# Optimization experiments

Measured on AMD Instinct MI355X. Metric: run time of the kernel, lower is better.

## Reference

```python
import jax, jax.numpy as jnp
import numpy as np

K = 8       # out_caps
H = 64      # nhidden
TAU = 1.0

def _l2norm(x, eps=1e-12):
    n = jnp.linalg.norm(x, axis=-1, keepdims=True)
    return x / jnp.maximum(n, eps)

def setup_inputs() -> dict:
    key = jax.random.key(0)
    k1, k2, k3, k4 = jax.random.split(key, 4)
    B, N, NB, D = 128, 50, 32, K * H
    return {
        "self_vectors": jax.random.normal(k1, (B, N, D), dtype=jnp.float32),
        "neighbor_vectors": jax.random.normal(k2, (B, N, NB, D), dtype=jnp.float32),
        "W1": jax.random.normal(k3, (D, D), dtype=jnp.float32) * 0.04,
        "b1": jax.random.normal(k4, (D,), dtype=jnp.float32) * 0.01,
        "max_iter": 3,
    }

def reference(self_vectors, neighbor_vectors, W1, b1, max_iter):
    B, N, _ = self_vectors.shape
    NB = neighbor_vectors.shape[2]
    # fc1 + ReLU projections (dropout p=0 -> identity)
    self_z = jax.nn.relu(self_vectors @ W1.T + b1)            # [B,N,K*H]
    neigh_z = jax.nn.relu(neighbor_vectors @ W1.T + b1)       # [B,N,NB,K*H]
    s = _l2norm(self_z.reshape(B, N, K, H))                   # [B,N,K,H]
    nz = _l2norm(neigh_z.reshape(B, N, NB, K, H))             # [B,N,NB,K,H]
    u = None
    for it in range(max_iter):
        if u is None:
            p = jnp.zeros((B, N, NB, K), dtype=s.dtype)
        else:
            p = jnp.einsum('bnmkh,bnkh->bnmk', nz, u)
        p = jax.nn.softmax(p / TAU, axis=-1)                   # softmax over K
        u = jnp.einsum('bnmkh,bnmk->bnkh', nz, p) + s          # sum over neighbors
        if it < max_iter - 1:
            u = _l2norm(u)
    return jax.nn.relu(u.reshape(B, N, K * H))
```

## Files before the change

### kernel.cpp

```cpp
#include <hip/hip_runtime.h>
#include <hip/hip_bf16.h>


#define D_DIM 512
#define BM 64
#define BK 32
#define KSTEPS 16

typedef __attribute__((ext_vector_type(8))) short short8;
typedef __attribute__((ext_vector_type(4))) short short4v;
typedef __attribute__((ext_vector_type(4))) float f32x4;

static __device__ __forceinline__ short f2bf(float f) {
    __bf16 b = (__bf16)f;
    return __builtin_bit_cast(short, b);
}
static __device__ __forceinline__ float bf2f(short s) {
    unsigned u = ((unsigned)(unsigned short)s) << 16;
    return __builtin_bit_cast(float, u);
}
static __device__ __forceinline__ void gload_lds16(const void* g, void* l) {
    __builtin_amdgcn_global_load_lds(
        (const __attribute__((address_space(1))) void*)g,
        (__attribute__((address_space(3))) void*)l, 16, 0, 0);
}

__global__ __launch_bounds__(256) void wconv(const float* __restrict__ W,
                                             short* __restrict__ Wb) {
    const int i = (blockIdx.x * 256 + threadIdx.x) * 8;
    const float4 v0 = *reinterpret_cast<const float4*>(W + i);
    const float4 v1 = *reinterpret_cast<const float4*>(W + i + 4);
    short8 o;
    o[0] = f2bf(v0.x); o[1] = f2bf(v0.y); o[2] = f2bf(v0.z); o[3] = f2bf(v0.w);
    o[4] = f2bf(v1.x); o[5] = f2bf(v1.y); o[6] = f2bf(v1.z); o[7] = f2bf(v1.w);
    *reinterpret_cast<short8*>(Wb + i) = o;
}

template <bool FUSED>
__global__ __launch_bounds__(256, 2) void gemm_route(
    const float* __restrict__ A,
    const short* __restrict__ Wb,
    const float* __restrict__ bias,
    short* __restrict__ Zs,
    const short* __restrict__ S,
    const int* __restrict__ miter_ptr,
    float* __restrict__ out)
{
    __shared__ __align__(16) char smem[81920];
    float* const lAf32 = (float*)smem;
    short* const lB = (short*)(smem + 16384);

    const int t = threadIdx.x;
    const int lane = t & 63;
    const int wid = t >> 6;
    const size_t row0 = (size_t)blockIdx.x * BM;
    const int wc = wid * 128;

    const int cb = wc + (lane & 15);
    float bcol[8];
    #pragma unroll
    for (int n = 0; n < 8; ++n) bcol[n] = bias[cb + n * 16];
    int miter = 0;
    if (FUSED) miter = *miter_ptr;

    auto stage = [&](int step, int buf) {
        const int k0 = (step < KSTEPS ? step : 0) * BK;
        #pragma unroll
        for (int i = 0; i < 8; ++i) {
            const int c = wid * 8 + i;
            const int r = c * 16 + (lane >> 2);
            const int g = ((lane & 3) - (r >> 1)) & 3;
            gload_lds16(Wb + (size_t)r * D_DIM + k0 + g * 8,
                        lB + buf * 16384 + c * 512);
        }
        #pragma unroll
        for (int i = 0; i < 2; ++i) {
            const int c = wid * 2 + i;
            const int r = c * 8 + (lane >> 3);
            const int g = ((lane & 7) - 2 * (r & 3)) & 7;
            gload_lds16(A + (row0 + r) * D_DIM + k0 + g * 4,
                        lAf32 + buf * 2048 + c * 256);
        }
    };

    f32x4 acc[4][8] = {};
    auto compute = [&](int buf) {
        const int q = lane >> 4;
        short8 af[4], bfr[8];
        #pragma unroll
        for (int m = 0; m < 4; ++m) {
            const int r = m * 16 + (lane & 15);
            const float* ap = lAf32 + buf * 2048 + r * 32 + ((q + (r & 3)) & 3) * 8;
            const f32x4 a0 = *reinterpret_cast<const f32x4*>(ap);
            const f32x4 a1 = *reinterpret_cast<const f32x4*>(ap + 4);
            short8 f;
            f[0] = f2bf(a0[0]); f[1] = f2bf(a0[1]);
            f[2] = f2bf(a0[2]); f[3] = f2bf(a0[3]);
            f[4] = f2bf(a1[0]); f[5] = f2bf(a1[1]);
            f[6] = f2bf(a1[2]); f[7] = f2bf(a1[3]);
            af[m] = f;
        }
        #pragma unroll
        for (int n = 0; n < 8; ++n) {
            const int r = wc + n * 16 + (lane & 15);
            bfr[n] = *reinterpret_cast<const short8*>(
                lB + buf * 16384 + r * 32 + ((q + (r >> 1)) & 3) * 8);
        }
        #pragma unroll
        for (int m = 0; m < 4; ++m)
            #pragma unroll
            for (int n = 0; n < 8; ++n)
                acc[m][n] = __builtin_amdgcn_mfma_f32_16x16x32_bf16(
                    af[m], bfr[n], acc[m][n], 0, 0, 0);
    };

    stage(0, 0);
    stage(1, 1);
    asm volatile("s_waitcnt vmcnt(10)" ::: "memory");
    __builtin_amdgcn_s_barrier();
    #pragma unroll
    for (int tk = 0; tk < KSTEPS; ++tk) {
        compute(tk & 1);
        asm volatile("s_waitcnt lgkmcnt(0)" ::: "memory");
        __builtin_amdgcn_s_barrier();
        stage(tk + 2, tk & 1);
        asm volatile("s_waitcnt vmcnt(10)" ::: "memory");
        __builtin_amdgcn_s_barrier();
    }
    asm volatile("s_waitcnt vmcnt(0)" ::: "memory");
    __builtin_amdgcn_s_barrier();

    short* const zbuf = (short*)(smem + 16384);
    #pragma unroll
    for (int m = 0; m < 4; ++m) {
        #pragma unroll
        for (int r = 0; r < 4; ++r) {
            float v[8];
            float ssa = 0.0f, ssb = 0.0f;
            #pragma unroll
            for (int n = 0; n < 4; ++n) {
                v[n] = fmaxf(acc[m][n][r] + bcol[n], 0.0f);
                ssa = fmaf(v[n], v[n], ssa);
            }
            #pragma unroll
            for (int n = 4; n < 8; ++n) {
                v[n] = fmaxf(acc[m][n][r] + bcol[n], 0.0f);
                ssb = fmaf(v[n], v[n], ssb);
            }
            ssa += __shfl_xor(ssa, 1); ssb += __shfl_xor(ssb, 1);
            ssa += __shfl_xor(ssa, 2); ssb += __shfl_xor(ssb, 2);
            ssa += __shfl_xor(ssa, 4); ssb += __shfl_xor(ssb, 4);
            ssa += __shfl_xor(ssa, 8); ssb += __shfl_xor(ssb, 8);
            const float inva = 1.0f / fmaxf(sqrtf(ssa), 1e-12f);
            const float invb = 1.0f / fmaxf(sqrtf(ssb), 1e-12f);
            const int orow = m * 16 + (lane >> 4) * 4 + r;
            if (FUSED) {
                #pragma unroll
                for (int n = 0; n < 4; ++n)
                    zbuf[orow * D_DIM + cb + n * 16] = f2bf(v[n] * inva);
                #pragma unroll
                for (int n = 4; n < 8; ++n)
                    zbuf[orow * D_DIM + cb + n * 16] = f2bf(v[n] * invb);
            } else {
                #pragma unroll
                for (int n = 0; n < 4; ++n)
                    Zs[(row0 + orow) * D_DIM + cb + n * 16] = f2bf(v[n] * inva);
                #pragma unroll
                for (int n = 4; n < 8; ++n)
                    Zs[(row0 + orow) * D_DIM + cb + n * 16] = f2bf(v[n] * invb);
            }
        }
    }

    if (!FUSED) return;
    __syncthreads();

    float* const scratch = (float*)smem;
    const int tt = t & 127;
    const int ssid = t >> 7;
    const size_t site = (size_t)blockIdx.x * 2 + ssid;
    float* const u_ = scratch + ssid * 512;
    float* const p_ = (float*)(smem + 4096) + ssid * 256;
    const short* const zr = zbuf + ssid * 32 * D_DIM;

    const int e = tt * 4;
    const int go = tt >> 4;
    const short4v sv = *reinterpret_cast<const short4v*>(S + site * D_DIM + e);
    const float s0 = bf2f(sv[0]), s1 = bf2f(sv[1]);
    const float s2 = bf2f(sv[2]), s3 = bf2f(sv[3]);

    float v0, v1, v2, v3;
    {
        float a0 = 0, a1 = 0, a2 = 0, a3 = 0;
        for (int m = 0; m < 32; ++m) {
            const short4v z = *reinterpret_cast<const short4v*>(zr + m * D_DIM + e);
            a0 += bf2f(z[0]); a1 += bf2f(z[1]); a2 += bf2f(z[2]); a3 += bf2f(z[3]);
        }
        v0 = fmaf(a0, 0.125f, s0); v1 = fmaf(a1, 0.125f, s1);
        v2 = fmaf(a2, 0.125f, s2); v3 = fmaf(a3, 0.125f, s3);
    }

    const int dm = tt >> 2;
    const int ka = (tt & 3) * 2;

    for (int it = 1; it < miter; ++it) {
        float ssum = v0 * v0 + v1 * v1 + v2 * v2 + v3 * v3;
        ssum += __shfl_xor(ssum, 1);
        ssum += __shfl_xor(ssum, 2);
        ssum += __shfl_xor(ssum, 4);
        ssum += __shfl_xor(ssum, 8);
        const float inv = 1.0f / fmaxf(sqrtf(ssum), 1e-12f);
        v0 *= inv; v1 *= inv; v2 *= inv; v3 *= inv;
        *reinterpret_cast<float4*>(u_ + e) = make_float4(v0, v1, v2, v3);
        __syncthreads();

        const short* const za = zr + dm * D_DIM + ka * 64;
        const float* const ua = u_ + ka * 64;
        float da = 0, db = 0;
        #pragma unroll
        for (int j = 0; j < 8; ++j) {
            const int jj = ((j + (tt & 7)) & 7) * 8;
            const short8 zva = *reinterpret_cast<const short8*>(za + jj);
            const short8 zvb = *reinterpret_cast<const short8*>(za + 64 + jj);
            const f32x4 uA0 = *reinterpret_cast<const f32x4*>(ua + jj);
            const f32x4 uA1 = *reinterpret_cast<const f32x4*>(ua + jj + 4);
            const f32x4 uB0 = *reinterpret_cast<const f32x4*>(ua + 64 + jj);
            const f32x4 uB1 = *reinterpret_cast<const f32x4*>(ua + 64 + jj + 4);
            #pragma unroll
            for (int qq = 0; qq < 4; ++qq) {
                da = fmaf(bf2f(zva[qq]), uA0[qq], da);
                da = fmaf(bf2f(zva[qq + 4]), uA1[qq], da);
                db = fmaf(bf2f(zvb[qq]), uB0[qq], db);
                db = fmaf(bf2f(zvb[qq + 4]), uB1[qq], db);
            }
        }
        float mx = fmaxf(da, db);
        mx = fmaxf(mx, __shfl_xor(mx, 1));
        mx = fmaxf(mx, __shfl_xor(mx, 2));
        const float ea = __expf(da - mx), eb = __expf(db - mx);
        float sm_ = ea + eb;
        sm_ += __shfl_xor(sm_, 1);
        sm_ += __shfl_xor(sm_, 2);
        const float rs = 1.0f / sm_;
        *reinterpret_cast<float2*>(p_ + dm * 8 + ka) = make_float2(ea * rs, eb * rs);
        __syncthreads();

        float a0 = 0, a1 = 0, a2 = 0, a3 = 0;
        for (int m = 0; m < 32; ++m) {
            const short4v z = *reinterpret_cast<const short4v*>(zr + m * D_DIM + e);
            const float pm = p_[m * 8 + go];
            a0 = fmaf(bf2f(z[0]), pm, a0); a1 = fmaf(bf2f(z[1]), pm, a1);
            a2 = fmaf(bf2f(z[2]), pm, a2); a3 = fmaf(bf2f(z[3]), pm, a3);
        }
        v0 = s0 + a0; v1 = s1 + a1; v2 = s2 + a2; v3 = s3 + a3;
    }

    *reinterpret_cast<float4*>(out + site * D_DIM + e) =
        make_float4(fmaxf(v0, 0.0f), fmaxf(v1, 0.0f),
                    fmaxf(v2, 0.0f), fmaxf(v3, 0.0f));
}

extern "C" void kernel_launch(void* const* d_in, const int* in_sizes, int n_in,
                              void* d_out, int out_size, void* d_ws, size_t ws_size,
                              hipStream_t stream) {
    const float* self_v  = (const float*)d_in[0];
    const float* neigh_v = (const float*)d_in[1];
    const float* W1      = (const float*)d_in[2];
    const float* b1      = (const float*)d_in[3];
    const int*   miter   = (const int*)d_in[4];
    float* out = (float*)d_out;

    const int sites = in_sizes[0] / D_DIM;
    const int nrows = in_sizes[1] / D_DIM;

    short* s  = (short*)d_ws;
    short* Wb = s + (size_t)sites * D_DIM;

    wconv<<<dim3(D_DIM * D_DIM / (256 * 8)), dim3(256), 0, stream>>>(W1, Wb);
    gemm_route<false><<<dim3(sites / BM), dim3(256), 0, stream>>>(
        self_v, Wb, b1, s, nullptr, nullptr, nullptr);
    gemm_route<true><<<dim3(nrows / BM), dim3(256), 0, stream>>>(
        neigh_v, Wb, b1, nullptr, s, miter, out);
}
```

Baseline: 250.5 us.

## Load GEMM operands directly into registers instead of staging through LDS

Drops the async global-to-LDS double-buffered staging of the A tile and the bf16 weights. Each lane now loads its MFMA fragments straight from global memory into a two-deep register buffer, prefetching the next K step while the current one computes. This removes LDS traffic, the swizzle arithmetic and the per-step barriers, and shrinks shared memory. In exchange it raises register pressure, duplicates global reads of W across blocks and waves with no LDS sharing, and uses less coalesced global access patterns.

```diff
diff --git a/kernel.cpp b/kernel.cpp
--- a/kernel.cpp
+++ b/kernel.cpp
@@ -4,7 +4,6 @@
 
 #define D_DIM 512
 #define BM 64
-#define BK 32
 #define KSTEPS 16
 
 typedef __attribute__((ext_vector_type(8))) short short8;
@@ -18,11 +17,6 @@
 static __device__ __forceinline__ float bf2f(short s) {
     unsigned u = ((unsigned)(unsigned short)s) << 16;
     return __builtin_bit_cast(float, u);
-}
-static __device__ __forceinline__ void gload_lds16(const void* g, void* l) {
-    __builtin_amdgcn_global_load_lds(
-        (const __attribute__((address_space(1))) void*)g,
-        (__attribute__((address_space(3))) void*)l, 16, 0, 0);
 }
 
 __global__ __launch_bounds__(256) void wconv(const float* __restrict__ W,
@@ -46,9 +40,7 @@
     const int* __restrict__ miter_ptr,
     float* __restrict__ out)
 {
-    __shared__ __align__(16) char smem[81920];
-    float* const lAf32 = (float*)smem;
-    short* const lB = (short*)(smem + 16384);
+    __shared__ __align__(16) char smem[71680];
 
     const int t = threadIdx.x;
     const int lane = t & 63;
@@ -63,74 +55,51 @@
     int miter = 0;
     if (FUSED) miter = *miter_ptr;
 
-    auto stage = [&](int step, int buf) {
-        const int k0 = (step < KSTEPS ? step : 0) * BK;
-        #pragma unroll
-        for (int i = 0; i < 8; ++i) {
-            const int c = wid * 8 + i;
-            const int r = c * 16 + (lane >> 2);
-            const int g = ((lane & 3) - (r >> 1)) & 3;
-            gload_lds16(Wb + (size_t)r * D_DIM + k0 + g * 8,
-                        lB + buf * 16384 + c * 512);
-        }
-        #pragma unroll
-        for (int i = 0; i < 2; ++i) {
-            const int c = wid * 2 + i;
-            const int r = c * 8 + (lane >> 3);
-            const int g = ((lane & 7) - 2 * (r & 3)) & 7;
-            gload_lds16(A + (row0 + r) * D_DIM + k0 + g * 4,
-                        lAf32 + buf * 2048 + c * 256);
-        }
+    const float* const aBase = A + (row0 + (lane & 15)) * D_DIM + (lane >> 4) * 8;
+    const short* const bBase = Wb + (size_t)(wc + (lane & 15)) * D_DIM + (lane >> 4) * 8;
+
+    float4 aR[2][8];
+    short8 bR[2][8];
+
+    auto loadStep = [&](int k0, int buf) {
+        #pragma unroll
+        for (int m = 0; m < 4; ++m) {
+            const float* p = aBase + m * 16 * D_DIM + k0;
+            aR[buf][2 * m]     = *reinterpret_cast<const float4*>(p);
+            aR[buf][2 * m + 1] = *reinterpret_cast<const float4*>(p + 4);
+        }
+        #pragma unroll
+        for (int n = 0; n < 8; ++n)
+            bR[buf][n] = *reinterpret_cast<const short8*>(bBase + n * 16 * D_DIM + k0);
     };
 
     f32x4 acc[4][8] = {};
-    auto compute = [&](int buf) {
-        const int q = lane >> 4;
-        short8 af[4], bfr[8];
+
+    loadStep(0, 0);
+    #pragma unroll
+    for (int tk = 0; tk < KSTEPS; ++tk) {
+        const int cur = tk & 1;
+        short8 af[4];
         #pragma unroll
         for (int m = 0; m < 4; ++m) {
-            const int r = m * 16 + (lane & 15);
-            const float* ap = lAf32 + buf * 2048 + r * 32 + ((q + (r & 3)) & 3) * 8;
-            const f32x4 a0 = *reinterpret_cast<const f32x4*>(ap);
-            const f32x4 a1 = *reinterpret_cast<const f32x4*>(ap + 4);
             short8 f;
-            f[0] = f2bf(a0[0]); f[1] = f2bf(a0[1]);
-            f[2] = f2bf(a0[2]); f[3] = f2bf(a0[3]);
-            f[4] = f2bf(a1[0]); f[5] = f2bf(a1[1]);
-            f[6] = f2bf(a1[2]); f[7] = f2bf(a1[3]);
+            #pragma unroll
+            for (int j = 0; j < 4; ++j) {
+                f[j]     = f2bf(aR[cur][2 * m][j]);
+                f[4 + j] = f2bf(aR[cur][2 * m + 1][j]);
+            }
             af[m] = f;
         }
-        #pragma unroll
-        for (int n = 0; n < 8; ++n) {
-            const int r = wc + n * 16 + (lane & 15);
-            bfr[n] = *reinterpret_cast<const short8*>(
-                lB + buf * 16384 + r * 32 + ((q + (r >> 1)) & 3) * 8);
-        }
+        if (tk < KSTEPS - 1) loadStep((tk + 1) * 32, cur ^ 1);
         #pragma unroll
         for (int m = 0; m < 4; ++m)
             #pragma unroll
             for (int n = 0; n < 8; ++n)
                 acc[m][n] = __builtin_amdgcn_mfma_f32_16x16x32_bf16(
-                    af[m], bfr[n], acc[m][n], 0, 0, 0);
-    };
-
-    stage(0, 0);
-    stage(1, 1);
-    asm volatile("s_waitcnt vmcnt(10)" ::: "memory");
-    __builtin_amdgcn_s_barrier();
-    #pragma unroll
-    for (int tk = 0; tk < KSTEPS; ++tk) {
-        compute(tk & 1);
-        asm volatile("s_waitcnt lgkmcnt(0)" ::: "memory");
-        __builtin_amdgcn_s_barrier();
-        stage(tk + 2, tk & 1);
-        asm volatile("s_waitcnt vmcnt(10)" ::: "memory");
-        __builtin_amdgcn_s_barrier();
-    }
-    asm volatile("s_waitcnt vmcnt(0)" ::: "memory");
-    __builtin_amdgcn_s_barrier();
-
-    short* const zbuf = (short*)(smem + 16384);
+                    af[m], bR[cur][n], acc[m][n], 0, 0, 0);
+    }
+
+    short* const zbuf = (short*)smem;
     #pragma unroll
     for (int m = 0; m < 4; ++m) {
         #pragma unroll
@@ -175,12 +144,11 @@
     if (!FUSED) return;
     __syncthreads();
 
-    float* const scratch = (float*)smem;
     const int tt = t & 127;
     const int ssid = t >> 7;
     const size_t site = (size_t)blockIdx.x * 2 + ssid;
-    float* const u_ = scratch + ssid * 512;
-    float* const p_ = (float*)(smem + 4096) + ssid * 256;
+    float* const u_ = (float*)(smem + 65536) + ssid * 512;
+    float* const p_ = (float*)(smem + 69632) + ssid * 256;
     const short* const zr = zbuf + ssid * 32 * D_DIM;
 
     const int e = tt * 4;
```

Result: slower. 552.7 us (+120.6%).

## Keep normalized neighbor projections in MFMA registers for routing instead of LDS

Applied to the files above, without the earlier changes.

The routing epilogue used to write the normalized bf16 projections to shared memory and re-read them in every iteration. It now keeps the fp32 normalized values in the MFMA accumulator registers. Dot products and weighted sums are done with wave shuffles, and only the routing logits go through LDS for the softmax. The change also raises wave priority around the MFMA block. This removes LDS round-trips and bf16 rounding of the projections, but adds shuffle reductions, a serial 64-thread softmax step and more barriers.

```diff
diff --git a/kernel.cpp b/kernel.cpp
--- a/kernel.cpp
+++ b/kernel.cpp
@@ -8,7 +8,6 @@
 #define KSTEPS 16
 
 typedef __attribute__((ext_vector_type(8))) short short8;
-typedef __attribute__((ext_vector_type(4))) short short4v;
 typedef __attribute__((ext_vector_type(4))) float f32x4;
 
 static __device__ __forceinline__ short f2bf(float f) {
@@ -55,8 +54,10 @@
     const int wid = t >> 6;
     const size_t row0 = (size_t)blockIdx.x * BM;
     const int wc = wid * 128;
-
-    const int cb = wc + (lane & 15);
+    const int l15 = lane & 15;
+    const int q = lane >> 4;
+
+    const int cb = wc + l15;
     float bcol[8];
     #pragma unroll
     for (int n = 0; n < 8; ++n) bcol[n] = bias[cb + n * 16];
@@ -85,12 +86,12 @@
 
     f32x4 acc[4][8] = {};
     auto compute = [&](int buf) {
-        const int q = lane >> 4;
+        const int sq = lane >> 4;
         short8 af[4], bfr[8];
         #pragma unroll
         for (int m = 0; m < 4; ++m) {
-            const int r = m * 16 + (lane & 15);
-            const float* ap = lAf32 + buf * 2048 + r * 32 + ((q + (r & 3)) & 3) * 8;
+            const int r = m * 16 + l15;
+            const float* ap = lAf32 + buf * 2048 + r * 32 + ((sq + (r & 3)) & 3) * 8;
             const f32x4 a0 = *reinterpret_cast<const f32x4*>(ap);
             const f32x4 a1 = *reinterpret_cast<const f32x4*>(ap + 4);
             short8 f;
@@ -102,16 +103,18 @@
         }
         #pragma unroll
         for (int n = 0; n < 8; ++n) {
-            const int r = wc + n * 16 + (lane & 15);
+            const int r = wc + n * 16 + l15;
             bfr[n] = *reinterpret_cast<const short8*>(
-                lB + buf * 16384 + r * 32 + ((q + (r >> 1)) & 3) * 8);
-        }
+                lB + buf * 16384 + r * 32 + ((sq + (r >> 1)) & 3) * 8);
+        }
+        __builtin_amdgcn_s_setprio(1);
         #pragma unroll
         for (int m = 0; m < 4; ++m)
             #pragma unroll
             for (int n = 0; n < 8; ++n)
                 acc[m][n] = __builtin_amdgcn_mfma_f32_16x16x32_bf16(
                     af[m], bfr[n], acc[m][n], 0, 0, 0);
+        __builtin_amdgcn_s_setprio(0);
     };
 
     stage(0, 0);
@@ -130,7 +133,6 @@
     asm volatile("s_waitcnt vmcnt(0)" ::: "memory");
     __builtin_amdgcn_s_barrier();
 
-    short* const zbuf = (short*)(smem + 16384);
     #pragma unroll
     for (int m = 0; m < 4; ++m) {
         #pragma unroll
@@ -153,15 +155,13 @@
             ssa += __shfl_xor(ssa, 8); ssb += __shfl_xor(ssb, 8);
             const float inva = 1.0f / fmaxf(sqrtf(ssa), 1e-12f);
             const float invb = 1.0f / fmaxf(sqrtf(ssb), 1e-12f);
-            const int orow = m * 16 + (lane >> 4) * 4 + r;
             if (FUSED) {
                 #pragma unroll
-                for (int n = 0; n < 4; ++n)
-                    zbuf[orow * D_DIM + cb + n * 16] = f2bf(v[n] * inva);
-                #pragma unroll
-                for (int n = 4; n < 8; ++n)
-                    zbuf[orow * D_DIM + cb + n * 16] = f2bf(v[n] * invb);
+                for (int n = 0; n < 4; ++n) acc[m][n][r] = v[n] * inva;
+                #pragma unroll
+                for (int n = 4; n < 8; ++n) acc[m][n][r] = v[n] * invb;
             } else {
+                const int orow = m * 16 + q * 4 + r;
                 #pragma unroll
                 for (int n = 0; n < 4; ++n)
                     Zs[(row0 + orow) * D_DIM + cb + n * 16] = f2bf(v[n] * inva);
@@ -173,91 +173,127 @@
     }
 
     if (!FUSED) return;
-    __syncthreads();
-
-    float* const scratch = (float*)smem;
-    const int tt = t & 127;
-    const int ssid = t >> 7;
-    const size_t site = (size_t)blockIdx.x * 2 + ssid;
-    float* const u_ = scratch + ssid * 512;
-    float* const p_ = (float*)(smem + 4096) + ssid * 256;
-    const short* const zr = zbuf + ssid * 32 * D_DIM;
-
-    const int e = tt * 4;
-    const int go = tt >> 4;
-    const short4v sv = *reinterpret_cast<const short4v*>(S + site * D_DIM + e);
-    const float s0 = bf2f(sv[0]), s1 = bf2f(sv[1]);
-    const float s2 = bf2f(sv[2]), s3 = bf2f(sv[3]);
-
-    float v0, v1, v2, v3;
+
+    float* const praw = (float*)smem;
+    const size_t site0 = (size_t)blockIdx.x * 2;
+
+    float sreg[2][8];
+    #pragma unroll
+    for (int st = 0; st < 2; ++st)
+        #pragma unroll
+        for (int n = 0; n < 8; ++n)
+            sreg[st][n] = bf2f(S[(site0 + st) * D_DIM + cb + n * 16]);
+
+    float u[2][8];
+    #pragma unroll
+    for (int st = 0; st < 2; ++st)
+        #pragma unroll
+        for (int n = 0; n < 8; ++n) {
+            float c = 0.0f;
+            #pragma unroll
+            for (int mi = 2 * st; mi < 2 * st + 2; ++mi)
+                #pragma unroll
+                for (int r = 0; r < 4; ++r) c += acc[mi][n][r];
+            c += __shfl_xor(c, 16);
+            c += __shfl_xor(c, 32);
+            u[st][n] = fmaf(c, 0.125f, sreg[st][n]);
+        }
+
+    for (int it = 1; it < miter; ++it) {
+        #pragma unroll
+        for (int st = 0; st < 2; ++st)
+            #pragma unroll
+            for (int g = 0; g < 2; ++g) {
+                float ss = 0.0f;
+                #pragma unroll
+                for (int n = 4 * g; n < 4 * g + 4; ++n)
+                    ss = fmaf(u[st][n], u[st][n], ss);
+                ss += __shfl_xor(ss, 1);
+                ss += __shfl_xor(ss, 2);
+                ss += __shfl_xor(ss, 4);
+                ss += __shfl_xor(ss, 8);
+                const float inv = 1.0f / fmaxf(sqrtf(ss), 1e-12f);
+                #pragma unroll
+                for (int n = 4 * g; n < 4 * g + 4; ++n) u[st][n] *= inv;
+            }
+
+        float pd0 = 0.0f, pd1 = 0.0f;
+        #pragma unroll
+        for (int mi = 0; mi < 4; ++mi)
+            #pragma unroll
+            for (int r = 0; r < 4; ++r) {
+                const int st = mi >> 1;
+                float d0 = 0.0f, d1 = 0.0f;
+                #pragma unroll
+                for (int n = 0; n < 4; ++n) {
+                    d0 = fmaf(acc[mi][n][r], u[st][n], d0);
+                    d1 = fmaf(acc[mi][n + 4][r], u[st][n + 4], d1);
+                }
+                d0 += __shfl_xor(d0, 1); d1 += __shfl_xor(d1, 1);
+                d0 += __shfl_xor(d0, 2); d1 += __shfl_xor(d1, 2);
+                d0 += __shfl_xor(d0, 4); d1 += __shfl_xor(d1, 4);
+                d0 += __shfl_xor(d0, 8); d1 += __shfl_xor(d1, 8);
+                if (l15 == mi * 4 + r) { pd0 = d0; pd1 = d1; }
+            }
+        {
+            const int site_w = l15 >> 3;
+            const int m_w = ((l15 >> 2) & 1) * 16 + q * 4 + (l15 & 3);
+            praw[(site_w * 32 + m_w) * 8 + 2 * wid]     = pd0;
+            praw[(site_w * 32 + m_w) * 8 + 2 * wid + 1] = pd1;
+        }
+        __syncthreads();
+
+        if (t < 64) {
+            float* pr = praw + t * 8;
+            float mx = pr[0];
+            #pragma unroll
+            for (int k = 1; k < 8; ++k) mx = fmaxf(mx, pr[k]);
+            float sum = 0.0f;
+            float e[8];
+            #pragma unroll
+            for (int k = 0; k < 8; ++k) { e[k] = __expf(pr[k] - mx); sum += e[k]; }
+            const float rs = 1.0f / sum;
+            #pragma unroll
+            for (int k = 0; k < 8; ++k) pr[k] = e[k] * rs;
+        }
+        __syncthreads();
+
+        float cacc[2][8] = {};
+        #pragma unroll
+        for (int mi = 0; mi < 4; ++mi)
+            #pragma unroll
+            for (int r = 0; r < 4; ++r) {
+                const int st = mi >> 1;
+                const int m_w = (mi & 1) * 16 + q * 4 + r;
+                const float p0 = praw[(st * 32 + m_w) * 8 + 2 * wid];
+                const float p1 = praw[(st * 32 + m_w) * 8 + 2 * wid + 1];
+                #pragma unroll
+                for (int n = 0; n < 4; ++n) {
+                    cacc[st][n]     = fmaf(acc[mi][n][r],     p0, cacc[st][n]);
+                    cacc[st][n + 4] = fmaf(acc[mi][n + 4][r], p1, cacc[st][n + 4]);
+                }
+            }
+        #pragma unroll
+        for (int st = 0; st < 2; ++st)
+            #pragma unroll
+            for (int n = 0; n < 8; ++n) {
+                float c = cacc[st][n];
+                c += __shfl_xor(c, 16);
+                c += __shfl_xor(c, 32);
+                u[st][n] = sreg[st][n] + c;
+            }
+        __syncthreads();
+    }
+
     {
-        float a0 = 0, a1 = 0, a2 = 0, a3 = 0;
-        for (int m = 0; m < 32; ++m) {
-            const short4v z = *reinterpret_cast<const short4v*>(zr + m * D_DIM + e);
-            a0 += bf2f(z[0]); a1 += bf2f(z[1]); a2 += bf2f(z[2]); a3 += bf2f(z[3]);
-        }
-        v0 = fmaf(a0, 0.125f, s0); v1 = fmaf(a1, 0.125f, s1);
-        v2 = fmaf(a2, 0.125f, s2); v3 = fmaf(a3, 0.125f, s3);
+        const int st = q & 1;
+        const int nb = (q >> 1) * 4;
+        #pragma unroll
+        for (int j = 0; j < 4; ++j) {
+            const int n = nb + j;
+            out[(site0 + st) * D_DIM + cb + n * 16] = fmaxf(u[st][n], 0.0f);
+        }
     }
-
-    const int dm = tt >> 2;
-    const int ka = (tt & 3) * 2;
-
-    for (int it = 1; it < miter; ++it) {
-        float ssum = v0 * v0 + v1 * v1 + v2 * v2 + v3 * v3;
-        ssum += __shfl_xor(ssum, 1);
-        ssum += __shfl_xor(ssum, 2);
-        ssum += __shfl_xor(ssum, 4);
-        ssum += __shfl_xor(ssum, 8);
-        const float inv = 1.0f / fmaxf(sqrtf(ssum), 1e-12f);
-        v0 *= inv; v1 *= inv; v2 *= inv; v3 *= inv;
-        *reinterpret_cast<float4*>(u_ + e) = make_float4(v0, v1, v2, v3);
-        __syncthreads();
-
-        const short* const za = zr + dm * D_DIM + ka * 64;
-        const float* const ua = u_ + ka * 64;
-        float da = 0, db = 0;
-        #pragma unroll
-        for (int j = 0; j < 8; ++j) {
-            const int jj = ((j + (tt & 7)) & 7) * 8;
-            const short8 zva = *reinterpret_cast<const short8*>(za + jj);
-            const short8 zvb = *reinterpret_cast<const short8*>(za + 64 + jj);
-            const f32x4 uA0 = *reinterpret_cast<const f32x4*>(ua + jj);
-            const f32x4 uA1 = *reinterpret_cast<const f32x4*>(ua + jj + 4);
-            const f32x4 uB0 = *reinterpret_cast<const f32x4*>(ua + 64 + jj);
-            const f32x4 uB1 = *reinterpret_cast<const f32x4*>(ua + 64 + jj + 4);
-            #pragma unroll
-            for (int qq = 0; qq < 4; ++qq) {
-                da = fmaf(bf2f(zva[qq]), uA0[qq], da);
-                da = fmaf(bf2f(zva[qq + 4]), uA1[qq], da);
-                db = fmaf(bf2f(zvb[qq]), uB0[qq], db);
-                db = fmaf(bf2f(zvb[qq + 4]), uB1[qq], db);
-            }
-        }
-        float mx = fmaxf(da, db);
-        mx = fmaxf(mx, __shfl_xor(mx, 1));
-        mx = fmaxf(mx, __shfl_xor(mx, 2));
-        const float ea = __expf(da - mx), eb = __expf(db - mx);
-        float sm_ = ea + eb;
-        sm_ += __shfl_xor(sm_, 1);
-        sm_ += __shfl_xor(sm_, 2);
-        const float rs = 1.0f / sm_;
-        *reinterpret_cast<float2*>(p_ + dm * 8 + ka) = make_float2(ea * rs, eb * rs);
-        __syncthreads();
-
-        float a0 = 0, a1 = 0, a2 = 0, a3 = 0;
-        for (int m = 0; m < 32; ++m) {
-            const short4v z = *reinterpret_cast<const short4v*>(zr + m * D_DIM + e);
-            const float pm = p_[m * 8 + go];
-            a0 = fmaf(bf2f(z[0]), pm, a0); a1 = fmaf(bf2f(z[1]), pm, a1);
-            a2 = fmaf(bf2f(z[2]), pm, a2); a3 = fmaf(bf2f(z[3]), pm, a3);
-        }
-        v0 = s0 + a0; v1 = s1 + a1; v2 = s2 + a2; v3 = s3 + a3;
-    }
-
-    *reinterpret_cast<float4*>(out + site * D_DIM + e) =
-        make_float4(fmaxf(v0, 0.0f), fmaxf(v1, 0.0f),
-                    fmaxf(v2, 0.0f), fmaxf(v3, 0.0f));
 }
 
 extern "C" void kernel_launch(void* const* d_in, const int* in_sizes, int n_in,
```

Result: slower. 457.7 us (+82.7%).
